# Kernel optimization log

Measured on AMD Instinct MI355X. Metric: run time of the kernel, lower is better.

Reference implementation:

```python
import jax, jax.numpy as jnp
import numpy as np

L_X, L_D = 10, 4
T_N, T_F = 0.0, 1.0
C_BG = (1.0, 1.0, 1.0)


def _pe(p, L):
    # NeRF positional encoding: [sin(2^i pi p), cos(2^i pi p)] for i in 0..L-1
    freqs = (2.0 ** jnp.arange(L, dtype=p.dtype)) * jnp.pi  # [L]
    ang = p[..., None, :] * freqs[:, None]  # [..., L, 3]
    enc = jnp.concatenate([jnp.sin(ang), jnp.cos(ang)], axis=-1)  # [..., L, 6]
    return enc.reshape(p.shape[:-1] + (6 * L,))


def setup_inputs() -> dict:
    key = jax.random.key(0)
    ks = jax.random.split(key, 16)
    B, N, H, HL = 2048, 128, 256, 128
    Dx, Dd = 6 * L_X, 6 * L_D  # 60, 24
    o = jax.random.normal(ks[0], (B, 3), dtype=jnp.float32) * 0.5
    d = jax.random.normal(ks[1], (B, 3), dtype=jnp.float32)
    d = d / jnp.linalg.norm(d, axis=-1, keepdims=True)
    # stratified coarse samples in [t_n, t_f] (sorted by construction)
    u = jax.random.uniform(ks[2], (B, N), dtype=jnp.float32)
    t = T_N + (T_F - T_N) * ((jnp.arange(N, dtype=jnp.float32) / N)[None, :] + u / N)
    w = lambda k, fi, fo: jax.random.normal(k, (fi, fo), dtype=jnp.float32) * jnp.sqrt(2.0 / fi)
    Wh = jax.random.normal(ks[4], (4, H, H), dtype=jnp.float32) * jnp.sqrt(2.0 / H)
    return dict(
        o=o, d=d, t=t,
        W0=w(ks[3], Dx, H), b0=jnp.zeros((H,), jnp.float32),
        Wh=Wh, bh=jnp.zeros((4, H), jnp.float32),
        W5=w(ks[5], H + Dx, H), b5=jnp.zeros((H,), jnp.float32),
        W6=w(ks[6], H, H), b6=jnp.zeros((H,), jnp.float32),
        W7=w(ks[7], H, H), b7=jnp.zeros((H,), jnp.float32),
        Ws=w(ks[8], H, 1), bs=jnp.zeros((1,), jnp.float32),
        Wf=w(ks[9], H, H), bf=jnp.zeros((H,), jnp.float32),
        Wm=w(ks[10], H + Dd, HL), bm=jnp.zeros((HL,), jnp.float32),
        Wr=w(ks[11], HL, 3), br=jnp.zeros((3,), jnp.float32),
    )


def _forward(o, d, t, W0, b0, Wh, bh, W5, b5, W6, b6, W7, b7, Ws, bs, Wf, bf, Wm, bm, Wr, br):
    B, N = t.shape
    # sample points along rays: x = o + t * d  -> [B, N, 3]
    x = o[:, None, :] + t[..., None] * d[:, None, :]
    px = _pe(x, L_X).reshape(B * N, -1)            # [BN, 60]
    pd = _pe(d, L_D)                               # [B, 24]
    pd = jnp.broadcast_to(pd[:, None, :], (B, N, pd.shape[-1])).reshape(B * N, -1)
    # radiance field MLP (standard NeRF trunk with skip at layer 5)
    h = jax.nn.relu(px @ W0 + b0)
    for i in range(4):
        h = jax.nn.relu(h @ Wh[i] + bh[i])
    h = jnp.concatenate([h, px], axis=-1)
    h = jax.nn.relu(h @ W5 + b5)
    h = jax.nn.relu(h @ W6 + b6)
    h = jax.nn.relu(h @ W7 + b7)
    sigma = jax.nn.relu(h @ Ws + bs).reshape(B, N)  # density
    feat = h @ Wf + bf
    h2 = jax.nn.relu(jnp.concatenate([feat, pd], axis=-1) @ Wm + bm)
    rgb = jax.nn.sigmoid(h2 @ Wr + br).reshape(B, N, 3)
    # volume rendering weights (matches torch pad/exp/cumsum logic)
    delta = jnp.concatenate([t[:, 1:] - t[:, :-1], jnp.full((B, 1), 1e8, t.dtype)], axis=1)
    mass = sigma * delta                             # [B, N]
    mass0 = jnp.concatenate([jnp.zeros((B, 1), t.dtype), mass], axis=1)
    alpha = 1.0 - jnp.exp(-mass0[:, 1:])
    T = jnp.exp(-jnp.cumsum(mass0[:, :-1], axis=1))
    wgt = T * alpha                                  # [B, N]
    C = jnp.sum(wgt[..., None] * rgb, axis=1)        # [B, 3]
    bg = jnp.asarray(C_BG, dtype=C.dtype)[None, :]
    C = C + (1.0 - jnp.sum(wgt, axis=1, keepdims=True)) * bg
    return C


def reference(o, d, t, W0, b0, Wh, bh, W5, b5, W6, b6, W7, b7, Ws, bs, Wf, bf, Wm, bm, Wr, br):
    return _forward(o, d, t, W0, b0, Wh, bh, W5, b5, W6, b6, W7, b7, Ws, bs, Wf, bf, Wm, bm, Wr, br)
```

## Files before the change

### kernel.cpp

```cpp
#include <hip/hip_runtime.h>
#include <hip/hip_fp16.h>
#include <math.h>

typedef __bf16 bf16x8 __attribute__((ext_vector_type(8)));
typedef float  f32x4  __attribute__((ext_vector_type(4)));

#define AH  264
#define TOT 589824

#define OFF_W0T   0
#define OFF_WHT   16384
#define OFF_W5AT  278528
#define OFF_W5BT  344064
#define OFF_W6T   360448
#define OFF_W7T   425984
#define OFF_WFT   491520
#define OFF_WMAT  557056

__global__ void prep_weights(const float* __restrict__ W0, const float* __restrict__ Wh,
                             const float* __restrict__ W5, const float* __restrict__ W6,
                             const float* __restrict__ W7, const float* __restrict__ Wf,
                             const float* __restrict__ Wm, __bf16* __restrict__ ws) {
  int idx = blockIdx.x * blockDim.x + threadIdx.x;
  if (idx >= TOT) return;
  float v = 0.f;
  if (idx < OFF_WHT)        { int j = idx;            int n=j>>6, k=j&63;   v = (k<60)? W0[k*256+n] : 0.f; }
  else if (idx < OFF_W5AT)  { int j = idx - OFF_WHT;  int i=j>>16, r=j&65535, n=r>>8, k=r&255; v = Wh[i*65536+k*256+n]; }
  else if (idx < OFF_W5BT)  { int j = idx - OFF_W5AT; int n=j>>8, k=j&255;  v = W5[k*256+n]; }
  else if (idx < OFF_W6T)   { int j = idx - OFF_W5BT; int n=j>>6, k=j&63;   v = (k<60)? W5[(256+k)*256+n] : 0.f; }
  else if (idx < OFF_W7T)   { int j = idx - OFF_W6T;  int n=j>>8, k=j&255;  v = W6[k*256+n]; }
  else if (idx < OFF_WFT)   { int j = idx - OFF_W7T;  int n=j>>8, k=j&255;  v = W7[k*256+n]; }
  else if (idx < OFF_WMAT)  { int j = idx - OFF_WFT;  int n=j>>8, k=j&255;  v = Wf[k*256+n]; }
  else                      { int j = idx - OFF_WMAT; int n=j>>8, k=j&255;  v = Wm[k*128+n]; }
  __bf16 hi = (__bf16)v;
  ws[idx] = hi;
  ws[TOT + idx] = (__bf16)(v - (float)hi);
}

template<int NT, int HALF>
__device__ void mfma_layer(__bf16* aHi, __bf16* aLo, const __half* pxh,
    const __bf16* __restrict__ wHi, const __bf16* __restrict__ wLo, int kStr, int nkc,
    const __bf16* __restrict__ xHi, const __bf16* __restrict__ xLo,
    const float* __restrict__ bias, const float* __restrict__ pdW,
    bool relu, int tid) {
  const int wave = tid >> 6, lane = tid & 63;
  const int lm = lane & 15, kq = lane >> 4;
  const int mBase = HALF ? 0 : (wave >> 2) * 64;
  const int nBase = (HALF ? wave : (wave & 3)) * (NT * 16);
  f32x4 acc[4][NT];
#pragma unroll
  for (int mt = 0; mt < 4; ++mt)
#pragma unroll
    for (int nt = 0; nt < NT; ++nt)
#pragma unroll
      for (int e = 0; e < 4; ++e) acc[mt][nt][e] = 0.f;

  for (int kc = 0; kc < nkc; ++kc) {
    const int kb = kc*32 + kq*8;
    bf16x8 ah[4], al[4], bh[NT], bl[NT];
#pragma unroll
    for (int mt = 0; mt < 4; ++mt) {
      const int off = (mBase + mt*16 + lm)*AH + kb;
      ah[mt] = *(const bf16x8*)(aHi + off);
      al[mt] = *(const bf16x8*)(aLo + off);
    }
#pragma unroll
    for (int nt = 0; nt < NT; ++nt) {
      const int ro = (nBase + nt*16 + lm)*kStr + kb;
      bh[nt] = *(const bf16x8*)(wHi + ro);
      bl[nt] = *(const bf16x8*)(wLo + ro);
    }
#pragma unroll
    for (int p = 0; p < 3; ++p)
#pragma unroll
      for (int mt = 0; mt < 4; ++mt)
#pragma unroll
        for (int nt = 0; nt < NT; ++nt)
          acc[mt][nt] = __builtin_amdgcn_mfma_f32_16x16x32_bf16(
              (p == 2) ? al[mt] : ah[mt],
              (p == 1) ? bl[nt] : bh[nt],
              acc[mt][nt], 0, 0, 0);
  }
  if (xHi) {
#pragma unroll
    for (int kc = 0; kc < 2; ++kc) {
      const int kb = kc*32 + kq*8;
      bf16x8 ah[4], al[4], bh[NT], bl[NT];
#pragma unroll
      for (int mt = 0; mt < 4; ++mt) {
        const __half* pr = pxh + (mBase + mt*16 + lm)*64 + kb;
#pragma unroll
        for (int j = 0; j < 8; ++j) {
          float v = __half2float(pr[j]);
          __bf16 h = (__bf16)v;
          ah[mt][j] = h;
          al[mt][j] = (__bf16)(v - (float)h);
        }
      }
#pragma unroll
      for (int nt = 0; nt < NT; ++nt) {
        const int ro = (nBase + nt*16 + lm)*64 + kb;
        bh[nt] = *(const bf16x8*)(xHi + ro);
        bl[nt] = *(const bf16x8*)(xLo + ro);
      }
#pragma unroll
      for (int p = 0; p < 3; ++p)
#pragma unroll
        for (int mt = 0; mt < 4; ++mt)
#pragma unroll
          for (int nt = 0; nt < NT; ++nt)
            acc[mt][nt] = __builtin_amdgcn_mfma_f32_16x16x32_bf16(
                (p == 2) ? al[mt] : ah[mt],
                (p == 1) ? bl[nt] : bh[nt],
                acc[mt][nt], 0, 0, 0);
    }
  }
  __syncthreads();
#pragma unroll
  for (int mt = 0; mt < 4; ++mt)
#pragma unroll
    for (int nt = 0; nt < NT; ++nt) {
      const int col = nBase + nt*16 + lm;
      float bv = bias[col] + (pdW ? pdW[col] : 0.f);
#pragma unroll
      for (int r = 0; r < 4; ++r) {
        const int row = mBase + mt*16 + kq*4 + r;
        float v = acc[mt][nt][r] + bv;
        if (relu) v = fmaxf(v, 0.f);
        __bf16 h = (__bf16)v;
        aHi[row*AH + col] = h;
        aLo[row*AH + col] = (__bf16)(v - (float)h);
      }
    }
  __syncthreads();
}

template<int HALF>
__global__ __launch_bounds__(512, 4) void nerf_main(
    const float* __restrict__ ro, const float* __restrict__ rd, const float* __restrict__ tin,
    const float* __restrict__ b0, const float* __restrict__ bh,
    const float* __restrict__ b5, const float* __restrict__ b6,
    const float* __restrict__ b7,
    const float* __restrict__ Wsig, const float* __restrict__ bs,
    const float* __restrict__ bfb,
    const float* __restrict__ Wm, const float* __restrict__ bm,
    const float* __restrict__ Wr, const float* __restrict__ br,
    const __bf16* __restrict__ wsHi, const __bf16* __restrict__ wsLo,
    float* __restrict__ part, float* __restrict__ out) {
  constexpr int M = HALF ? 64 : 128;
  __shared__ __align__(16) __bf16 aHi[M * AH];
  __shared__ __align__(16) __bf16 aLo[M * AH];
  __shared__ __align__(16) unsigned char pxred[M * 128];
  __shared__ __align__(16) float  pdBuf[24];
  __shared__ __align__(16) float  pdW[128];
  __shared__ __align__(16) float  tBuf[M + 4];
  __shared__ __align__(16) float  sigBuf[M];
  __shared__ __align__(16) float  rgbBuf[M * 3];

  __half* pxh = (__half*)pxred;
  float*  red = (float*)pxred;

  const int blk  = blockIdx.x;
  const int ray  = HALF ? (blk >> 1) : blk;
  const int S    = HALF ? (blk & 1) * 64 : 0;
  const int tid  = threadIdx.x;

  if (tid < M) {
    const int m = tid;
    float tv = tin[ray*128 + S + m];
    tBuf[m] = tv;
    float xs[3];
#pragma unroll
    for (int c = 0; c < 3; ++c) xs[c] = ro[ray*3 + c] + tv * rd[ray*3 + c];
#pragma unroll
    for (int i = 0; i < 10; ++i)
#pragma unroll
      for (int c = 0; c < 3; ++c) {
        float a = ldexpf(xs[c], i);
        pxh[m*64 + i*6 + c]     = __float2half(sinpif(a));
        pxh[m*64 + i*6 + 3 + c] = __float2half(cospif(a));
      }
#pragma unroll
    for (int j = 60; j < 64; ++j) pxh[m*64 + j] = __float2half(0.f);
  } else if (tid < M + 24) {
    int j = tid - M;
    int i = j / 6, r = j % 6;
    float a = ldexpf(rd[ray*3 + (r % 3)], i);
    pdBuf[j] = (r < 3) ? sinpif(a) : cospif(a);
  } else if (tid == M + 24) {
    tBuf[M] = (S + M < 128) ? tin[ray*128 + S + M] : 0.f;
  }
  __syncthreads();
  if (tid >= 256 && tid < 384) {
    int c = tid - 256;
    float s = 0.f;
#pragma unroll
    for (int j = 0; j < 24; ++j) s += pdBuf[j] * Wm[(256 + j)*128 + c];
    pdW[c] = s;
  }
  __syncthreads();

  constexpr int NTF = HALF ? 2 : 4;
  constexpr int NTW = HALF ? 1 : 2;

  mfma_layer<NTF, HALF>(aHi, aLo, pxh, nullptr, nullptr, 0, 0,
                        wsHi + OFF_W0T, wsLo + OFF_W0T, b0, nullptr, true, tid);
  for (int i = 0; i < 4; ++i)
    mfma_layer<NTF, HALF>(aHi, aLo, pxh, wsHi + OFF_WHT + i*65536, wsLo + OFF_WHT + i*65536, 256, 8,
                          nullptr, nullptr, bh + i*256, nullptr, true, tid);
  mfma_layer<NTF, HALF>(aHi, aLo, pxh, wsHi + OFF_W5AT, wsLo + OFF_W5AT, 256, 8,
                        wsHi + OFF_W5BT, wsLo + OFF_W5BT, b5, nullptr, true, tid);
  mfma_layer<NTF, HALF>(aHi, aLo, pxh, wsHi + OFF_W6T, wsLo + OFF_W6T, 256, 8,
                        nullptr, nullptr, b6, nullptr, true, tid);
  mfma_layer<NTF, HALF>(aHi, aLo, pxh, wsHi + OFF_W7T, wsLo + OFF_W7T, 256, 8,
                        nullptr, nullptr, b7, nullptr, true, tid);

  {
    constexpr int TPS = 512 / M;
    const int m = tid / TPS, q = tid % TPS;
    const int kn = 256 / TPS;
    float s = 0.f;
    for (int k = q*kn; k < q*kn + kn; ++k)
      s += ((float)aHi[m*AH + k] + (float)aLo[m*AH + k]) * Wsig[k];
    red[tid] = s;
    __syncthreads();
    if (tid < M) {
      float sm = bs[0];
#pragma unroll
      for (int j = 0; j < TPS; ++j) sm += red[TPS*tid + j];
      sigBuf[tid] = fmaxf(sm, 0.f);
    }
    __syncthreads();
  }

  mfma_layer<NTF, HALF>(aHi, aLo, nullptr, wsHi + OFF_WFT, wsLo + OFF_WFT, 256, 8,
                        nullptr, nullptr, bfb, nullptr, false, tid);

  mfma_layer<NTW, HALF>(aHi, aLo, nullptr, wsHi + OFF_WMAT, wsLo + OFF_WMAT, 256, 8,
                        nullptr, nullptr, bm, pdW, true, tid);

  {
    constexpr int TPS = 512 / M;
    const int m = tid / TPS, q = tid % TPS;
    const int kn = 128 / TPS;
    float r0s = 0.f, r1s = 0.f, r2s = 0.f;
    for (int k = q*kn; k < q*kn + kn; ++k) {
      float hv = (float)aHi[m*AH + k] + (float)aLo[m*AH + k];
      r0s += hv * Wr[k*3 + 0];
      r1s += hv * Wr[k*3 + 1];
      r2s += hv * Wr[k*3 + 2];
    }
    red[tid] = r0s; red[512 + tid] = r1s; red[1024 + tid] = r2s;
    __syncthreads();
    if (tid < M) {
#pragma unroll
      for (int c = 0; c < 3; ++c) {
        float sm = br[c];
#pragma unroll
        for (int j = 0; j < TPS; ++j) sm += red[c*512 + TPS*tid + j];
        rgbBuf[tid*3 + c] = 1.f / (1.f + expf(-sm));
      }
    }
    __syncthreads();
  }

  if (tid == 0) {
    float T = 1.f, c0 = 0.f, c1 = 0.f, c2 = 0.f, wsum = 0.f;
    for (int m = 0; m < M; ++m) {
      float delta = (S + m < 127) ? (tBuf[m + 1] - tBuf[m]) : 1e8f;
      float e = expf(-sigBuf[m] * delta);
      float w = T * (1.f - e);
      c0 += w * rgbBuf[m*3 + 0];
      c1 += w * rgbBuf[m*3 + 1];
      c2 += w * rgbBuf[m*3 + 2];
      wsum += w;
      T *= e;
    }
    if (HALF) {
      float* p = part + blk*5;
      p[0] = c0; p[1] = c1; p[2] = c2; p[3] = wsum; p[4] = T;
    } else {
      float bg = 1.f - wsum;
      out[ray*3 + 0] = c0 + bg;
      out[ray*3 + 1] = c1 + bg;
      out[ray*3 + 2] = c2 + bg;
    }
  }
}

__global__ void combine(const float* __restrict__ part, float* __restrict__ out) {
  int r = blockIdx.x * blockDim.x + threadIdx.x;
  if (r >= 2048) return;
  const float* p0 = part + (2*r)*5;
  const float* p1 = p0 + 5;
  float T0 = p0[4];
  float wsum = p0[3] + T0 * p1[3];
  float bg = 1.f - wsum;
#pragma unroll
  for (int c = 0; c < 3; ++c)
    out[r*3 + c] = p0[c] + T0 * p1[c] + bg;
}

extern "C" void kernel_launch(void* const* d_in, const int* in_sizes, int n_in,
                              void* d_out, int out_size, void* d_ws, size_t ws_size,
                              hipStream_t stream) {
  const float* ro  = (const float*)d_in[0];
  const float* rd  = (const float*)d_in[1];
  const float* t   = (const float*)d_in[2];
  const float* W0  = (const float*)d_in[3];
  const float* b0  = (const float*)d_in[4];
  const float* Wh  = (const float*)d_in[5];
  const float* bh  = (const float*)d_in[6];
  const float* W5  = (const float*)d_in[7];
  const float* b5  = (const float*)d_in[8];
  const float* W6  = (const float*)d_in[9];
  const float* b6  = (const float*)d_in[10];
  const float* W7  = (const float*)d_in[11];
  const float* b7  = (const float*)d_in[12];
  const float* Wsg = (const float*)d_in[13];
  const float* bs  = (const float*)d_in[14];
  const float* Wf  = (const float*)d_in[15];
  const float* bfb = (const float*)d_in[16];
  const float* Wm  = (const float*)d_in[17];
  const float* bm  = (const float*)d_in[18];
  const float* Wr  = (const float*)d_in[19];
  const float* br  = (const float*)d_in[20];
  float* out = (float*)d_out;

  __bf16* wsHi = (__bf16*)d_ws;
  __bf16* wsLo = wsHi + TOT;
  float*  part = (float*)((char*)d_ws + (size_t)2 * TOT * 2);

  const size_t needSplit = (size_t)2 * TOT * 2 + (size_t)4096 * 5 * 4;

  prep_weights<<<(TOT + 255)/256, 256, 0, stream>>>(W0, Wh, W5, W6, W7, Wf, Wm, wsHi);
  if (ws_size >= needSplit) {
    nerf_main<1><<<4096, 512, 0, stream>>>(ro, rd, t, b0, bh, b5, b6, b7,
                                           Wsg, bs, bfb, Wm, bm, Wr, br,
                                           wsHi, wsLo, part, out);
    combine<<<8, 256, 0, stream>>>(part, out);
  } else {
    nerf_main<0><<<2048, 512, 0, stream>>>(ro, rd, t, b0, bh, b5, b6, b7,
                                           Wsg, bs, bfb, Wm, bm, Wr, br,
                                           wsHi, wsLo, part, out);
  }
}
```

Measured before the change: 1.424 ms.

## Double-buffer weight fragments and interleave MFMA issue in NeRF MLP layers

For small-NT layers, the main GEMM loop now prefetches the next k-chunk of weight hi/lo fragments while computing the current one. A fragments are loaded in pairs of m-tiles just in time, which lowers the number of live registers. The skip-input path loads fp16 positional encodings as 8-wide vectors, and the sigma and rgb dot products read activations with vector LDS loads. Launch bounds now use amdgpu_waves_per_eu(4,4) to pin occupancy. The aim is to hide global weight-load latency and reduce register pressure, at the cost of more code and a separate branch for small NT.

```diff
diff --git a/kernel.cpp b/kernel.cpp
--- a/kernel.cpp
+++ b/kernel.cpp
@@ -2,8 +2,9 @@
 #include <hip/hip_fp16.h>
 #include <math.h>
 
-typedef __bf16 bf16x8 __attribute__((ext_vector_type(8)));
-typedef float  f32x4  __attribute__((ext_vector_type(4)));
+typedef __bf16   bf16x8 __attribute__((ext_vector_type(8)));
+typedef _Float16 f16x8  __attribute__((ext_vector_type(8)));
+typedef float    f32x4  __attribute__((ext_vector_type(4)));
 
 #define AH  264
 #define TOT 589824
@@ -37,6 +38,8 @@
   ws[TOT + idx] = (__bf16)(v - (float)hi);
 }
 
+#define MFMA16(A,B,C) __builtin_amdgcn_mfma_f32_16x16x32_bf16((A),(B),(C),0,0,0)
+
 template<int NT, int HALF>
 __device__ void mfma_layer(__bf16* aHi, __bf16* aLo, const __half* pxh,
     const __bf16* __restrict__ wHi, const __bf16* __restrict__ wLo, int kStr, int nkc,
@@ -55,48 +58,101 @@
 #pragma unroll
       for (int e = 0; e < 4; ++e) acc[mt][nt][e] = 0.f;
 
-  for (int kc = 0; kc < nkc; ++kc) {
-    const int kb = kc*32 + kq*8;
-    bf16x8 ah[4], al[4], bh[NT], bl[NT];
-#pragma unroll
-    for (int mt = 0; mt < 4; ++mt) {
-      const int off = (mBase + mt*16 + lm)*AH + kb;
-      ah[mt] = *(const bf16x8*)(aHi + off);
-      al[mt] = *(const bf16x8*)(aLo + off);
-    }
-#pragma unroll
-    for (int nt = 0; nt < NT; ++nt) {
-      const int ro = (nBase + nt*16 + lm)*kStr + kb;
-      bh[nt] = *(const bf16x8*)(wHi + ro);
-      bl[nt] = *(const bf16x8*)(wLo + ro);
-    }
-#pragma unroll
-    for (int p = 0; p < 3; ++p)
-#pragma unroll
-      for (int mt = 0; mt < 4; ++mt)
-#pragma unroll
-        for (int nt = 0; nt < NT; ++nt)
-          acc[mt][nt] = __builtin_amdgcn_mfma_f32_16x16x32_bf16(
-              (p == 2) ? al[mt] : ah[mt],
-              (p == 1) ? bl[nt] : bh[nt],
-              acc[mt][nt], 0, 0, 0);
+  if (nkc >= 2) {
+    if constexpr (NT <= 2) {
+      const int kb0 = kq * 8;
+      int wr[NT];
+#pragma unroll
+      for (int nt = 0; nt < NT; ++nt) wr[nt] = (nBase + nt*16 + lm)*kStr + kb0;
+      const int ab = (mBase + lm)*AH + kb0;
+      bf16x8 bhA[NT], blA[NT], bhB[NT], blB[NT];
+#pragma unroll
+      for (int nt = 0; nt < NT; ++nt) {
+        bhA[nt] = *(const bf16x8*)(wHi + wr[nt]);
+        blA[nt] = *(const bf16x8*)(wLo + wr[nt]);
+      }
+      for (int kc = 0; kc < nkc; kc += 2) {
+#pragma unroll
+        for (int nt = 0; nt < NT; ++nt) {
+          bhB[nt] = *(const bf16x8*)(wHi + wr[nt] + (kc+1)*32);
+          blB[nt] = *(const bf16x8*)(wLo + wr[nt] + (kc+1)*32);
+        }
+#pragma unroll
+        for (int mp = 0; mp < 2; ++mp) {
+          const int r0 = ab + mp*32*AH + kc*32;
+          bf16x8 a0h = *(const bf16x8*)(aHi + r0);
+          bf16x8 a0l = *(const bf16x8*)(aLo + r0);
+          bf16x8 a1h = *(const bf16x8*)(aHi + r0 + 16*AH);
+          bf16x8 a1l = *(const bf16x8*)(aLo + r0 + 16*AH);
+#pragma unroll
+          for (int nt = 0; nt < NT; ++nt) {
+            acc[2*mp  ][nt] = MFMA16(a0h, bhA[nt], acc[2*mp  ][nt]);
+            acc[2*mp+1][nt] = MFMA16(a1h, bhA[nt], acc[2*mp+1][nt]);
+            acc[2*mp  ][nt] = MFMA16(a0h, blA[nt], acc[2*mp  ][nt]);
+            acc[2*mp+1][nt] = MFMA16(a1h, blA[nt], acc[2*mp+1][nt]);
+            acc[2*mp  ][nt] = MFMA16(a0l, bhA[nt], acc[2*mp  ][nt]);
+            acc[2*mp+1][nt] = MFMA16(a1l, bhA[nt], acc[2*mp+1][nt]);
+          }
+        }
+        if (kc + 2 < nkc) {
+#pragma unroll
+          for (int nt = 0; nt < NT; ++nt) {
+            bhA[nt] = *(const bf16x8*)(wHi + wr[nt] + (kc+2)*32);
+            blA[nt] = *(const bf16x8*)(wLo + wr[nt] + (kc+2)*32);
+          }
+        }
+#pragma unroll
+        for (int mp = 0; mp < 2; ++mp) {
+          const int r0 = ab + mp*32*AH + (kc+1)*32;
+          bf16x8 a0h = *(const bf16x8*)(aHi + r0);
+          bf16x8 a0l = *(const bf16x8*)(aLo + r0);
+          bf16x8 a1h = *(const bf16x8*)(aHi + r0 + 16*AH);
+          bf16x8 a1l = *(const bf16x8*)(aLo + r0 + 16*AH);
+#pragma unroll
+          for (int nt = 0; nt < NT; ++nt) {
+            acc[2*mp  ][nt] = MFMA16(a0h, bhB[nt], acc[2*mp  ][nt]);
+            acc[2*mp+1][nt] = MFMA16(a1h, bhB[nt], acc[2*mp+1][nt]);
+            acc[2*mp  ][nt] = MFMA16(a0h, blB[nt], acc[2*mp  ][nt]);
+            acc[2*mp+1][nt] = MFMA16(a1h, blB[nt], acc[2*mp+1][nt]);
+            acc[2*mp  ][nt] = MFMA16(a0l, bhB[nt], acc[2*mp  ][nt]);
+            acc[2*mp+1][nt] = MFMA16(a1l, bhB[nt], acc[2*mp+1][nt]);
+          }
+        }
+      }
+    } else {
+      for (int kc = 0; kc < nkc; ++kc) {
+        const int kb = kc*32 + kq*8;
+        bf16x8 ah[4], al[4], bh[NT], bl[NT];
+#pragma unroll
+        for (int mt = 0; mt < 4; ++mt) {
+          const int off = (mBase + mt*16 + lm)*AH + kb;
+          ah[mt] = *(const bf16x8*)(aHi + off);
+          al[mt] = *(const bf16x8*)(aLo + off);
+        }
+#pragma unroll
+        for (int nt = 0; nt < NT; ++nt) {
+          const int ro = (nBase + nt*16 + lm)*kStr + kb;
+          bh[nt] = *(const bf16x8*)(wHi + ro);
+          bl[nt] = *(const bf16x8*)(wLo + ro);
+        }
+#pragma unroll
+        for (int p = 0; p < 3; ++p)
+#pragma unroll
+          for (int mt = 0; mt < 4; ++mt)
+#pragma unroll
+            for (int nt = 0; nt < NT; ++nt)
+              acc[mt][nt] = __builtin_amdgcn_mfma_f32_16x16x32_bf16(
+                  (p == 2) ? al[mt] : ah[mt],
+                  (p == 1) ? bl[nt] : bh[nt],
+                  acc[mt][nt], 0, 0, 0);
+      }
+    }
   }
   if (xHi) {
 #pragma unroll
     for (int kc = 0; kc < 2; ++kc) {
       const int kb = kc*32 + kq*8;
-      bf16x8 ah[4], al[4], bh[NT], bl[NT];
-#pragma unroll
-      for (int mt = 0; mt < 4; ++mt) {
-        const __half* pr = pxh + (mBase + mt*16 + lm)*64 + kb;
-#pragma unroll
-        for (int j = 0; j < 8; ++j) {
-          float v = __half2float(pr[j]);
-          __bf16 h = (__bf16)v;
-          ah[mt][j] = h;
-          al[mt][j] = (__bf16)(v - (float)h);
-        }
-      }
+      bf16x8 bh[NT], bl[NT];
 #pragma unroll
       for (int nt = 0; nt < NT; ++nt) {
         const int ro = (nBase + nt*16 + lm)*64 + kb;
@@ -104,15 +160,29 @@
         bl[nt] = *(const bf16x8*)(xLo + ro);
       }
 #pragma unroll
-      for (int p = 0; p < 3; ++p)
-#pragma unroll
-        for (int mt = 0; mt < 4; ++mt)
-#pragma unroll
-          for (int nt = 0; nt < NT; ++nt)
-            acc[mt][nt] = __builtin_amdgcn_mfma_f32_16x16x32_bf16(
-                (p == 2) ? al[mt] : ah[mt],
-                (p == 1) ? bl[nt] : bh[nt],
-                acc[mt][nt], 0, 0, 0);
+      for (int mp = 0; mp < 2; ++mp) {
+        bf16x8 ah[2], al[2];
+#pragma unroll
+        for (int i = 0; i < 2; ++i) {
+          const f16x8 pv = *(const f16x8*)((const _Float16*)pxh + (mBase + (2*mp+i)*16 + lm)*64 + kb);
+#pragma unroll
+          for (int j = 0; j < 8; ++j) {
+            float v = (float)pv[j];
+            __bf16 h = (__bf16)v;
+            ah[i][j] = h;
+            al[i][j] = (__bf16)(v - (float)h);
+          }
+        }
+#pragma unroll
+        for (int nt = 0; nt < NT; ++nt) {
+          acc[2*mp  ][nt] = MFMA16(ah[0], bh[nt], acc[2*mp  ][nt]);
+          acc[2*mp+1][nt] = MFMA16(ah[1], bh[nt], acc[2*mp+1][nt]);
+          acc[2*mp  ][nt] = MFMA16(ah[0], bl[nt], acc[2*mp  ][nt]);
+          acc[2*mp+1][nt] = MFMA16(ah[1], bl[nt], acc[2*mp+1][nt]);
+          acc[2*mp  ][nt] = MFMA16(al[0], bh[nt], acc[2*mp  ][nt]);
+          acc[2*mp+1][nt] = MFMA16(al[1], bh[nt], acc[2*mp+1][nt]);
+        }
+      }
     }
   }
   __syncthreads();
@@ -136,7 +206,8 @@
 }
 
 template<int HALF>
-__global__ __launch_bounds__(512, 4) void nerf_main(
+__global__ __launch_bounds__(512) __attribute__((amdgpu_waves_per_eu(4, 4)))
+void nerf_main(
     const float* __restrict__ ro, const float* __restrict__ rd, const float* __restrict__ tin,
     const float* __restrict__ b0, const float* __restrict__ bh,
     const float* __restrict__ b5, const float* __restrict__ b6,
@@ -220,8 +291,12 @@
     const int m = tid / TPS, q = tid % TPS;
     const int kn = 256 / TPS;
     float s = 0.f;
-    for (int k = q*kn; k < q*kn + kn; ++k)
-      s += ((float)aHi[m*AH + k] + (float)aLo[m*AH + k]) * Wsig[k];
+    for (int k8 = q*kn; k8 < q*kn + kn; k8 += 8) {
+      bf16x8 vh = *(const bf16x8*)(aHi + m*AH + k8);
+      bf16x8 vl = *(const bf16x8*)(aLo + m*AH + k8);
+#pragma unroll
+      for (int j = 0; j < 8; ++j) s += ((float)vh[j] + (float)vl[j]) * Wsig[k8 + j];
+    }
     red[tid] = s;
     __syncthreads();
     if (tid < M) {
@@ -244,11 +319,16 @@
     const int m = tid / TPS, q = tid % TPS;
     const int kn = 128 / TPS;
     float r0s = 0.f, r1s = 0.f, r2s = 0.f;
-    for (int k = q*kn; k < q*kn + kn; ++k) {
-      float hv = (float)aHi[m*AH + k] + (float)aLo[m*AH + k];
-      r0s += hv * Wr[k*3 + 0];
-      r1s += hv * Wr[k*3 + 1];
-      r2s += hv * Wr[k*3 + 2];
+    for (int k8 = q*kn; k8 < q*kn + kn; k8 += 8) {
+      bf16x8 vh = *(const bf16x8*)(aHi + m*AH + k8);
+      bf16x8 vl = *(const bf16x8*)(aLo + m*AH + k8);
+#pragma unroll
+      for (int j = 0; j < 8; ++j) {
+        float hv = (float)vh[j] + (float)vl[j];
+        r0s += hv * Wr[(k8 + j)*3 + 0];
+        r1s += hv * Wr[(k8 + j)*3 + 1];
+        r2s += hv * Wr[(k8 + j)*3 + 2];
+      }
     }
     red[tid] = r0s; red[512 + tid] = r1s; red[1024 + tid] = r2s;
     __syncthreads();
```

After: 1.329 ms. 1.07x faster.
